# Kernel tuning notes

Hardware: AMD Instinct MI355X
Metric: run time of the kernel (lower is better)

Reference implementation:

```python
import jax, jax.numpy as jnp
import numpy as np

K = 9  # 3x3 deformable kernel taps
N_ITER = 3  # class constant N=4 -> 3 deform iterations + final offset conv


def conv3x3(x, w):
    # x: [B,C,H,W], w: [O,I,3,3], stride 1, padding 1, no bias
    return jax.lax.conv_general_dilated(
        x, w, window_strides=(1, 1), padding='SAME',
        dimension_numbers=('NCHW', 'OIHW', 'NCHW'))


def bilinear_gather(x, py, px):
    # x: [B,C,H,W]; py,px: [B,K,H,W] float sampling coords; zero outside bounds.
    B, C, H, W = x.shape
    y0 = jnp.floor(py); x0 = jnp.floor(px)
    wy1 = py - y0; wy0 = 1.0 - wy1
    wx1 = px - x0; wx0 = 1.0 - wx1
    xf = x.reshape(B, C, H * W)

    def corner(yi, xi):
        valid = (yi >= 0) & (yi <= H - 1) & (xi >= 0) & (xi <= W - 1)
        yc = jnp.clip(yi, 0, H - 1).astype(jnp.int32)
        xc = jnp.clip(xi, 0, W - 1).astype(jnp.int32)
        idx = (yc * W + xc).reshape(B, 1, -1)  # [B,1,K*H*W]
        v = jnp.take_along_axis(xf, idx, axis=2).reshape(B, C, K, H, W)
        return v * valid.astype(x.dtype)[:, None]  # zero-pad out-of-bounds

    w00 = (wy0 * wx0)[:, None]; w01 = (wy0 * wx1)[:, None]
    w10 = (wy1 * wx0)[:, None]; w11 = (wy1 * wx1)[:, None]
    return (w00 * corner(y0, x0) + w01 * corner(y0, x0 + 1)
            + w10 * corner(y0 + 1, x0) + w11 * corner(y0 + 1, x0 + 1))


def deform_conv(x, offset, w):
    # x: [B,C,H,W], offset: [B,2*K,H,W] as (dy,dx) per tap, w: [O,I,3,3]
    B, C, H, W = x.shape
    off = offset.reshape(B, K, 2, H, W)
    ky = jnp.array([-1, -1, -1, 0, 0, 0, 1, 1, 1], dtype=x.dtype)
    kx = jnp.array([-1, 0, 1, -1, 0, 1, -1, 0, 1], dtype=x.dtype)
    py = off[:, :, 0] + ky[None, :, None, None] + jnp.arange(H, dtype=x.dtype)[None, None, :, None]
    px = off[:, :, 1] + kx[None, :, None, None] + jnp.arange(W, dtype=x.dtype)[None, None, None, :]
    v = bilinear_gather(x, py, px)  # [B,C,K,H,W]
    return jnp.einsum('bikhw,oik->bohw', v, w.reshape(w.shape[0], w.shape[1], K))


def setup_inputs() -> dict:
    key = jax.random.key(0)
    k1, k2, k3, k4 = jax.random.split(key, 4)
    B, C2, H, W = 4, 128, 64, 64
    in_ch = 2 * C2  # 256
    x = jax.random.normal(k1, (B, C2, H, W), dtype=jnp.float32)
    y = jax.random.normal(k2, (B, C2, H, W), dtype=jnp.float32)
    # small offset-conv weights so predicted offsets are modest (a few pixels)
    offset_w = jax.random.normal(k3, (4, 18, in_ch, 3, 3), dtype=jnp.float32) * 0.01
    deform_w = jax.random.normal(k4, (3, in_ch, in_ch, 3, 3), dtype=jnp.float32) * (1.0 / np.sqrt(in_ch * 9))
    return {'x': x, 'y': y, 'offset_w': offset_w, 'deform_w': deform_w}


def reference(x, y, offset_w, deform_w):
    feat = jnp.concatenate([x, y], axis=1)  # [B, 2C, H, W]
    for i in range(N_ITER):
        off = conv3x3(feat, offset_w[i])        # [B, 18, H, W]
        feat = deform_conv(feat, off, deform_w[i])
    return conv3x3(feat, offset_w[3])           # final offset field [B,18,H,W]
```

## Files before the change

### kernel.cpp

```cpp
#include <hip/hip_runtime.h>

typedef short short8 __attribute__((ext_vector_type(8)));
typedef float floatx4 __attribute__((ext_vector_type(4)));

constexpr int N_PIX  = 16384;
constexpr int FEAT_N = N_PIX * 256;
constexpr int OFF_N  = N_PIX * 18;
constexpr int KDIM   = 2304;
constexpr int WB_L   = 2304 * 256;
constexpr int WTO_L  = KDIM * 18;

__device__ __forceinline__ unsigned short bf16_rn(float v) {
  unsigned u = __float_as_uint(v);
  return (unsigned short)((u + 0x7FFFu + ((u >> 16) & 1u)) >> 16);
}
__device__ __forceinline__ void split_bf16(float v, short& h, short& l) {
  unsigned short hu = bf16_rn(v);
  float hf = __uint_as_float(((unsigned)hu) << 16);
  h = (short)hu;
  l = (short)bf16_rn(v - hf);
}

__global__ __launch_bounds__(256) void concat_nhwc(const float* __restrict__ x,
                                                   const float* __restrict__ y,
                                                   float* __restrict__ feat) {
  __shared__ float tile[64][65];
  int bid = blockIdx.x;
  int ct = bid & 3, h = (bid >> 2) & 63, b = bid >> 8;
  int c0 = ct * 64;
  const float* src = (c0 < 128) ? x : y;
  int cs = c0 & 127;
  int t = threadIdx.x;
  int w = t & 63, cl = t >> 6;
#pragma unroll
  for (int i = 0; i < 16; ++i) {
    int c = cl + i * 4;
    tile[c][w] = src[((b * 128 + cs + c) * 64 + h) * 64 + w];
  }
  __syncthreads();
  int c2 = t & 63, wl = t >> 6;
#pragma unroll
  for (int i = 0; i < 16; ++i) {
    int w2 = wl + i * 4;
    feat[((b * 64 + h) * 64 + w2) * 256 + c0 + c2] = tile[c2][w2];
  }
}

__global__ __launch_bounds__(256) void prep_wb(const float* __restrict__ dw,
                                               unsigned short* __restrict__ wbh,
                                               unsigned short* __restrict__ wbl) {
  int g = blockIdx.x * 256 + threadIdx.x;
  int l = g / WB_L, r = g % WB_L;
  int j = r & 7, lane = (r >> 3) & 63, nt = (r >> 9) & 15, kc = r >> 13;
  int k = kc * 32 + (lane >> 4) * 8 + j;
  int o = nt * 16 + (lane & 15);
  float w = dw[((l * 256 + o) * 256 + (k & 255)) * 9 + (k >> 8)];
  short h, lo; split_bf16(w, h, lo);
  wbh[g] = (unsigned short)h; wbl[g] = (unsigned short)lo;
}

__global__ __launch_bounds__(256) void t_ow(const float* __restrict__ ow,
                                            float* __restrict__ wto) {
  int g = blockIdx.x * 256 + threadIdx.x;
  int l = g / WTO_L, r = g % WTO_L;
  int o = r % 18, k = r / 18;
  int i = k & 255, tap = k >> 8;
  wto[g] = ow[(l * 18 + o) * KDIM + i * 9 + tap];
}

__global__ __launch_bounds__(256) void addf(float* __restrict__ a,
                                            const float* __restrict__ b) {
  int i = (blockIdx.x * 256 + threadIdx.x) * 4;
  float4 va = *(const float4*)(a + i);
  float4 vb = *(const float4*)(b + i);
  va.x += vb.x; va.y += vb.y; va.z += vb.z; va.w += vb.w;
  *(float4*)(a + i) = va;
}

template <bool NCHW>
__global__ __launch_bounds__(512) void off_conv(const float* __restrict__ feat,
                                                const float* __restrict__ wo,
                                                float* __restrict__ out) {
  __shared__ float red[512][19];
  int t = threadIdx.x;
  int lane = t & 63;
  int wid = __builtin_amdgcn_readfirstlane(t >> 6);
  const int bid = blockIdx.x;
  const int pg  = (bid & 7) * 32 + (bid >> 3);
  int p = pg * 64 + lane;
  int b = p >> 12, h = (p >> 6) & 63, w = p & 63;
  float acc[18] = {};
  for (int kc = wid * 18; kc < wid * 18 + 18; ++kc) {
    int k0 = kc * 16;
    int tap = k0 >> 8, c0 = k0 & 255;
    int y = h + tap / 3 - 1, xx = w + tap % 3 - 1;
    float a[16];
#pragma unroll
    for (int q = 0; q < 16; ++q) a[q] = 0.f;
    if ((unsigned)y < 64u && (unsigned)xx < 64u) {
      const float4* srcp =
          (const float4*)(feat + ((b * 64 + y) * 64 + xx) * 256 + c0);
#pragma unroll
      for (int q = 0; q < 4; ++q) {
        float4 v = srcp[q];
        a[q * 4 + 0] = v.x; a[q * 4 + 1] = v.y;
        a[q * 4 + 2] = v.z; a[q * 4 + 3] = v.w;
      }
    }
    const float* wp = wo + k0 * 18;
#pragma unroll
    for (int kk = 0; kk < 16; ++kk)
#pragma unroll
      for (int o = 0; o < 18; ++o)
        acc[o] += a[kk] * wp[kk * 18 + o];
  }
#pragma unroll
  for (int o = 0; o < 18; ++o) red[t][o] = acc[o];
  __syncthreads();
  if (t < 64) {
#pragma unroll
    for (int o = 0; o < 18; ++o) {
      float s = 0.f;
#pragma unroll
      for (int sg = 0; sg < 8; ++sg) s += red[lane + 64 * sg][o];
      if (NCHW)
        out[(b * 18 + o) * 4096 + (p & 4095)] = s;
      else
        out[p * 18 + o] = s;
    }
  }
}

__global__ __launch_bounds__(256) void deform_mfma(
    const float* __restrict__ feat, const float* __restrict__ off,
    const unsigned short* __restrict__ wbh, const unsigned short* __restrict__ wbl,
    float* __restrict__ out0, float* __restrict__ out1) {
  __shared__ __align__(16) unsigned short Ah[64 * 32], Al[64 * 32];
  __shared__ float cy[9][64], cx[9][64];
  const int t = threadIdx.x;
  const int r_  = blockIdx.x & 255;
  const int pg  = (r_ & 7) * 32 + (r_ >> 3);
  const int pbase = pg * 64;
  const int half  = blockIdx.x >> 8;
  const int bimg = pbase >> 12, h = (pbase >> 6) & 63;
  const float* fbase = feat + bimg * (4096 * 256);

  {
    int m = t & 63, p = pbase + m;
    for (int tap = t >> 6; tap < 9; tap += 4) {
      cy[tap][m] = off[p * 18 + 2 * tap]     + (float)(tap / 3 - 1 + h);
      cx[tap][m] = off[p * 18 + 2 * tap + 1] + (float)(tap % 3 - 1 + m);
    }
  }
  __syncthreads();

  const int m  = t & 63;
  const int cg = t >> 6;
  const int lane = t & 63;
  const int wv = __builtin_amdgcn_readfirstlane(t >> 6);
  const int awoff = ((m >> 4) * 64 + cg * 16 + (m & 15)) * 8;

  floatx4 acc[4][4];
  const floatx4 z4 = {0.f, 0.f, 0.f, 0.f};
#pragma unroll
  for (int i = 0; i < 4; ++i)
#pragma unroll
    for (int jn = 0; jn < 4; ++jn) acc[i][jn] = z4;

  int rowmap[4], colmap[4];
  {
    short8 cA, cB;
    int own = lane & 15, q = (lane >> 4) & 3;
#pragma unroll
    for (int j = 0; j < 8; ++j) {
      int k = q * 8 + j;
      cA[j] = (short)((k == own) ? bf16_rn(1.0f) : 0);
      cB[j] = (short)((k < 16) ? bf16_rn((float)(k * 16 + own)) : 0);
    }
    floatx4 cal = __builtin_amdgcn_mfma_f32_16x16x32_bf16(cA, cB, z4, 0, 0, 0);
#pragma unroll
    for (int r = 0; r < 4; ++r) {
      int v = (int)(cal[r] + 0.5f);
      rowmap[r] = (v >> 4) & 15;
      colmap[r] = v & 15;
    }
  }

  const short8* BH = (const short8*)wbh;
  const short8* BL = (const short8*)wbl;

  float4 pf[8];
  float w4[4];
  auto issue = [&](int kc) {
    int tap = kc >> 3, c0 = (kc & 7) * 32 + cg * 8;
    float py = cy[tap][m], px = cx[tap][m];
    float fy = floorf(py), fx = floorf(px);
    int iy = (int)fy, ix = (int)fx;
    float wy1 = py - fy, wx1 = px - fx;
    float wy0 = 1.f - wy1, wx0 = 1.f - wx1;
    w4[0] = wy0 * wx0; w4[1] = wy0 * wx1; w4[2] = wy1 * wx0; w4[3] = wy1 * wx1;
#pragma unroll
    for (int c = 0; c < 4; ++c) {
      int yy = iy + (c >> 1), xx = ix + (c & 1);
      bool ok = ((unsigned)yy < 64u) && ((unsigned)xx < 64u);
      if (!ok) w4[c] = 0.f;
      int yc = min(max(yy, 0), 63), xc = min(max(xx, 0), 63);
      const float4* p = (const float4*)(fbase + (yc * 64 + xc) * 256 + c0);
      pf[c * 2]     = p[0];
      pf[c * 2 + 1] = p[1];
    }
  };

  const int kcBeg = half * 36, kcEnd = kcBeg + 36;
  issue(kcBeg);
  for (int kc = kcBeg; kc < kcEnd; ++kc) {
    const float* pfp = (const float*)pf;
    short8 hv, lv;
#pragma unroll
    for (int j = 0; j < 8; ++j) {
      float v = w4[0] * pfp[j] + w4[1] * pfp[8 + j] + w4[2] * pfp[16 + j] +
                w4[3] * pfp[24 + j];
      short hh, ll; split_bf16(v, hh, ll);
      hv[j] = hh; lv[j] = ll;
    }
    __syncthreads();
    *(short8*)&Ah[awoff] = hv;
    *(short8*)&Al[awoff] = lv;
    __syncthreads();

    if (kc + 1 < kcEnd) issue(kc + 1);

    short8 ah[4], al[4], bh[4], bl[4];
#pragma unroll
    for (int mi = 0; mi < 4; ++mi) {
      ah[mi] = *(const short8*)&Ah[(mi * 64 + lane) * 8];
      al[mi] = *(const short8*)&Al[(mi * 64 + lane) * 8];
    }
#pragma unroll
    for (int ni = 0; ni < 4; ++ni) {
      int bidx = (kc * 16 + wv * 4 + ni) * 64 + lane;
      bh[ni] = BH[bidx];
      bl[ni] = BL[bidx];
    }
#pragma unroll
    for (int mi = 0; mi < 4; ++mi)
#pragma unroll
      for (int ni = 0; ni < 4; ++ni) {
        acc[mi][ni] = __builtin_amdgcn_mfma_f32_16x16x32_bf16(ah[mi], bh[ni], acc[mi][ni], 0, 0, 0);
        acc[mi][ni] = __builtin_amdgcn_mfma_f32_16x16x32_bf16(ah[mi], bl[ni], acc[mi][ni], 0, 0, 0);
        acc[mi][ni] = __builtin_amdgcn_mfma_f32_16x16x32_bf16(al[mi], bh[ni], acc[mi][ni], 0, 0, 0);
      }
  }

  float* o = half ? out1 : out0;
#pragma unroll
  for (int mi = 0; mi < 4; ++mi)
#pragma unroll
    for (int ni = 0; ni < 4; ++ni)
#pragma unroll
      for (int r = 0; r < 4; ++r) {
        int pgx = pbase + mi * 16 + rowmap[r];
        o[pgx * 256 + wv * 64 + ni * 16 + colmap[r]] = acc[mi][ni][r];
      }
}

extern "C" void kernel_launch(void* const* d_in, const int* in_sizes, int n_in,
                              void* d_out, int out_size, void* d_ws, size_t ws_size,
                              hipStream_t stream) {
  const float* x  = (const float*)d_in[0];
  const float* y  = (const float*)d_in[1];
  const float* ow = (const float*)d_in[2];
  const float* dw = (const float*)d_in[3];
  float* out = (float*)d_out;

  float* fA      = (float*)d_ws;
  float* fB      = fA + FEAT_N;
  float* off_buf = fB + FEAT_N;
  float* wto     = off_buf + OFF_N;
  unsigned short* wbh = (unsigned short*)(wto + 4 * WTO_L);
  unsigned short* wbl = wbh + 3 * WB_L;
  float* pscr    = (float*)(wbl + 3 * WB_L);

  concat_nhwc<<<dim3(1024), dim3(256), 0, stream>>>(x, y, fA);
  prep_wb<<<dim3(3 * WB_L / 256), dim3(256), 0, stream>>>(dw, wbh, wbl);
  t_ow<<<dim3(4 * WTO_L / 256), dim3(256), 0, stream>>>(ow, wto);

  float* cur = fA;
  float* nxt = fB;
  for (int i = 0; i < 3; ++i) {
    off_conv<false><<<dim3(256), dim3(512), 0, stream>>>(cur, wto + i * WTO_L,
                                                         off_buf);
    deform_mfma<<<dim3(512), dim3(256), 0, stream>>>(
        cur, off_buf, wbh + i * WB_L, wbl + i * WB_L, nxt, pscr);
    addf<<<dim3(FEAT_N / 4 / 256), dim3(256), 0, stream>>>(nxt, pscr);
    float* tmp = cur; cur = nxt; nxt = tmp;
  }
  off_conv<true><<<dim3(256), dim3(512), 0, stream>>>(cur, wto + 3 * WTO_L, out);
}
```

Measured before the change: 571.6 us.

## Split offset conv across K into three blocks and double-buffer deform MFMA staging

The offset convolution grid is tripled, with each block covering a third of the reduction dimension. A new kernel sums the three partial outputs, which is meant to raise occupancy on a grid that was only one block per CU. The deformable conv kernel now double-buffers its LDS A tiles and prefetches B fragments, halving barriers per k-step and overlapping gather/combine with MFMA. The cost is extra scratch memory traffic, an extra launch per offset conv, and more registers in the deform kernel.

After: 527.3 us. 1.08x faster.

```diff
diff --git a/kernel.cpp b/kernel.cpp
--- a/kernel.cpp
+++ b/kernel.cpp
@@ -76,21 +76,36 @@
   va.x += vb.x; va.y += vb.y; va.z += vb.z; va.w += vb.w;
   *(float4*)(a + i) = va;
 }
+__global__ __launch_bounds__(256) void addf2o(float* __restrict__ a,
+                                              const float* __restrict__ b,
+                                              const float* __restrict__ c) {
+  int i = (blockIdx.x * 256 + threadIdx.x) * 4;
+  float4 va = *(const float4*)(a + i);
+  float4 vb = *(const float4*)(b + i);
+  float4 vc = *(const float4*)(c + i);
+  va.x += vb.x + vc.x; va.y += vb.y + vc.y;
+  va.z += vb.z + vc.z; va.w += vb.w + vc.w;
+  *(float4*)(a + i) = va;
+}
 
 template <bool NCHW>
 __global__ __launch_bounds__(512) void off_conv(const float* __restrict__ feat,
                                                 const float* __restrict__ wo,
-                                                float* __restrict__ out) {
+                                                float* __restrict__ o0,
+                                                float* __restrict__ o1,
+                                                float* __restrict__ o2) {
   __shared__ float red[512][19];
   int t = threadIdx.x;
   int lane = t & 63;
   int wid = __builtin_amdgcn_readfirstlane(t >> 6);
-  const int bid = blockIdx.x;
-  const int pg  = (bid & 7) * 32 + (bid >> 3);
+  const int r_  = blockIdx.x & 255;
+  const int pg  = (r_ & 7) * 32 + (r_ >> 3);
+  const int third = blockIdx.x >> 8;
   int p = pg * 64 + lane;
   int b = p >> 12, h = (p >> 6) & 63, w = p & 63;
   float acc[18] = {};
-  for (int kc = wid * 18; kc < wid * 18 + 18; ++kc) {
+  const int cb = (third * 8 + wid) * 6;
+  for (int kc = cb; kc < cb + 6; ++kc) {
     int k0 = kc * 16;
     int tap = k0 >> 8, c0 = k0 & 255;
     int y = h + tap / 3 - 1, xx = w + tap % 3 - 1;
@@ -118,15 +133,16 @@
   for (int o = 0; o < 18; ++o) red[t][o] = acc[o];
   __syncthreads();
   if (t < 64) {
+    float* outp = (third == 0) ? o0 : (third == 1 ? o1 : o2);
 #pragma unroll
     for (int o = 0; o < 18; ++o) {
       float s = 0.f;
 #pragma unroll
       for (int sg = 0; sg < 8; ++sg) s += red[lane + 64 * sg][o];
       if (NCHW)
-        out[(b * 18 + o) * 4096 + (p & 4095)] = s;
+        outp[(b * 18 + o) * 4096 + (p & 4095)] = s;
       else
-        out[p * 18 + o] = s;
+        outp[p * 18 + o] = s;
     }
   }
 }
@@ -135,7 +151,7 @@
     const float* __restrict__ feat, const float* __restrict__ off,
     const unsigned short* __restrict__ wbh, const unsigned short* __restrict__ wbl,
     float* __restrict__ out0, float* __restrict__ out1) {
-  __shared__ __align__(16) unsigned short Ah[64 * 32], Al[64 * 32];
+  __shared__ __align__(16) unsigned short Ah[2][64 * 32], Al[2][64 * 32];
   __shared__ float cy[9][64], cx[9][64];
   const int t = threadIdx.x;
   const int r_  = blockIdx.x & 255;
@@ -210,10 +226,15 @@
       pf[c * 2 + 1] = p[1];
     }
   };
-
-  const int kcBeg = half * 36, kcEnd = kcBeg + 36;
-  issue(kcBeg);
-  for (int kc = kcBeg; kc < kcEnd; ++kc) {
+  auto loadB = [&](int kc, short8 (&bh)[4], short8 (&bl)[4]) {
+#pragma unroll
+    for (int ni = 0; ni < 4; ++ni) {
+      int bidx = (kc * 16 + wv * 4 + ni) * 64 + lane;
+      bh[ni] = BH[bidx];
+      bl[ni] = BL[bidx];
+    }
+  };
+  auto combine_stage = [&](int buf) {
     const float* pfp = (const float*)pf;
     short8 hv, lv;
 #pragma unroll
@@ -223,24 +244,15 @@
       short hh, ll; split_bf16(v, hh, ll);
       hv[j] = hh; lv[j] = ll;
     }
-    __syncthreads();
-    *(short8*)&Ah[awoff] = hv;
-    *(short8*)&Al[awoff] = lv;
-    __syncthreads();
-
-    if (kc + 1 < kcEnd) issue(kc + 1);
-
-    short8 ah[4], al[4], bh[4], bl[4];
+    *(short8*)&Ah[buf][awoff] = hv;
+    *(short8*)&Al[buf][awoff] = lv;
+  };
+  auto mfma16 = [&](int buf, const short8 (&bh)[4], const short8 (&bl)[4]) {
+    short8 ah[4], al[4];
 #pragma unroll
     for (int mi = 0; mi < 4; ++mi) {
-      ah[mi] = *(const short8*)&Ah[(mi * 64 + lane) * 8];
-      al[mi] = *(const short8*)&Al[(mi * 64 + lane) * 8];
-    }
-#pragma unroll
-    for (int ni = 0; ni < 4; ++ni) {
-      int bidx = (kc * 16 + wv * 4 + ni) * 64 + lane;
-      bh[ni] = BH[bidx];
-      bl[ni] = BL[bidx];
+      ah[mi] = *(const short8*)&Ah[buf][(mi * 64 + lane) * 8];
+      al[mi] = *(const short8*)&Al[buf][(mi * 64 + lane) * 8];
     }
 #pragma unroll
     for (int mi = 0; mi < 4; ++mi)
@@ -250,6 +262,29 @@
         acc[mi][ni] = __builtin_amdgcn_mfma_f32_16x16x32_bf16(ah[mi], bl[ni], acc[mi][ni], 0, 0, 0);
         acc[mi][ni] = __builtin_amdgcn_mfma_f32_16x16x32_bf16(al[mi], bh[ni], acc[mi][ni], 0, 0, 0);
       }
+  };
+
+  const int kcBeg = half * 36, kcEnd = kcBeg + 36;
+  short8 bhA[4], blA[4], bhB[4], blB[4];
+
+  issue(kcBeg);
+  combine_stage(0);
+  loadB(kcBeg, bhA, blA);
+  __syncthreads();
+
+  for (int kc = kcBeg; kc < kcEnd; kc += 2) {
+    issue(kc + 1);
+    loadB(kc + 1, bhB, blB);
+    mfma16(0, bhA, blA);
+    combine_stage(1);
+    __syncthreads();
+    if (kc + 2 < kcEnd) {
+      issue(kc + 2);
+      loadB(kc + 2, bhA, blA);
+    }
+    mfma16(1, bhB, blB);
+    if (kc + 2 < kcEnd) combine_stage(0);
+    __syncthreads();
   }
 
   float* o = half ? out1 : out0;
@@ -280,6 +315,8 @@
   unsigned short* wbh = (unsigned short*)(wto + 4 * WTO_L);
   unsigned short* wbl = wbh + 3 * WB_L;
   float* pscr    = (float*)(wbl + 3 * WB_L);
+  float* oscr1   = pscr + FEAT_N;
+  float* oscr2   = oscr1 + OFF_N;
 
   concat_nhwc<<<dim3(1024), dim3(256), 0, stream>>>(x, y, fA);
   prep_wb<<<dim3(3 * WB_L / 256), dim3(256), 0, stream>>>(dw, wbh, wbl);
@@ -288,12 +325,16 @@
   float* cur = fA;
   float* nxt = fB;
   for (int i = 0; i < 3; ++i) {
-    off_conv<false><<<dim3(256), dim3(512), 0, stream>>>(cur, wto + i * WTO_L,
-                                                         off_buf);
+    off_conv<false><<<dim3(768), dim3(512), 0, stream>>>(cur, wto + i * WTO_L,
+                                                         off_buf, oscr1, oscr2);
+    addf2o<<<dim3(OFF_N / 4 / 256), dim3(256), 0, stream>>>(off_buf, oscr1,
+                                                            oscr2);
     deform_mfma<<<dim3(512), dim3(256), 0, stream>>>(
         cur, off_buf, wbh + i * WB_L, wbl + i * WB_L, nxt, pscr);
     addf<<<dim3(FEAT_N / 4 / 256), dim3(256), 0, stream>>>(nxt, pscr);
     float* tmp = cur; cur = nxt; nxt = tmp;
   }
-  off_conv<true><<<dim3(256), dim3(512), 0, stream>>>(cur, wto + 3 * WTO_L, out);
-}
+  off_conv<true><<<dim3(768), dim3(512), 0, stream>>>(cur, wto + 3 * WTO_L, out,
+                                                      oscr1, oscr2);
+  addf2o<<<dim3(OFF_N / 4 / 256), dim3(256), 0, stream>>>(out, oscr1, oscr2);
+}
```
